# Performance work log

Measured on AMD Instinct MI355X. Metric: run time of the kernel, lower is better.

The kernel has to match this reference:

```python
import jax, jax.numpy as jnp
import numpy as np


def _mlp1(x, W, b):
    return jax.nn.relu(x @ W + b)


def _forward(battle_x, side_x, user_x, moveset_feat, movepool_feat, lookup_move_feat,
             lookup_move_mask, lastberry, lastberry_mask, items, abilities, types_x,
             tera_types_x, opt_moves, move_mask, can_tera, switch_mask,
             W_item, b_item, W_ab, b_ab, W_ms, b_ms, W_user, b_user,
             W_mo1, b_mo1, W_mo2, b_mo2, W_so1, b_so1, W_so2, b_so2,
             active_idx, switch_idx):
    B = battle_x.shape[0]
    # --- user block (vectorized over [B, 2 sides, 6 team members]) ---
    ms = _mlp1(moveset_feat, W_ms, b_ms)                    # [B,2,6,4,128]
    pool = _mlp1(movepool_feat, W_ms, b_ms).mean(axis=-2)   # [B,2,6,128] mean over move pool
    move_set_x = jnp.maximum(ms.max(axis=-2), pool)         # max over [4 slots + pool-mean]
    item_x = _mlp1(items, W_item, b_item).mean(axis=-2)     # [B,2,6,128]
    ability_x = _mlp1(abilities, W_ab, b_ab).mean(axis=-2)  # [B,2,6,128]
    # optional lookup slots: mask*relu(Wx+b) == zero vector when absent
    lk = _mlp1(lookup_move_feat, W_ms, b_ms) * lookup_move_mask[..., None]  # [B,2,6,5,128]
    berry = _mlp1(lastberry, W_item, b_item) * lastberry_mask[..., None]    # [B,2,6,128]
    lk_flat = lk.reshape(B, 2, 6, 5 * 128)
    u_in = jnp.concatenate([user_x, lk_flat, berry, move_set_x, item_x, ability_x,
                            types_x, tera_types_x], axis=-1)                # [B,2,6,1281]
    u = _mlp1(u_in, W_user, b_user)                                         # [B,2,6,512]
    # --- side block ---
    active = jnp.take_along_axis(u, active_idx[:, :, None, None], axis=2)[:, :, 0]  # [B,2,512]
    side_out = jnp.concatenate([side_x, active, u.max(axis=2)], axis=-1)    # [B,2,1041]
    battle_full = jnp.concatenate([battle_x, side_out[:, 0], side_out[:, 1]], axis=-1)  # [B,2091]
    D = battle_full.shape[-1]
    # --- move options: 4 moves x tera in {0,1} ---
    bt = jnp.broadcast_to(battle_full[:, None, None, :], (B, 4, 2, D))
    mv = jnp.broadcast_to(opt_moves[:, :, None, :], (B, 4, 2, 128))
    tera = jnp.broadcast_to(jnp.arange(2, dtype=battle_x.dtype)[None, None, :, None], (B, 4, 2, 1))
    xm = jnp.concatenate([bt, mv, tera], axis=-1)                           # [B,4,2,2220]
    mlogit = (_mlp1(xm, W_mo1, b_mo1) @ W_mo2 + b_mo2)[..., 0]              # [B,4,2]
    tera_ok = jnp.stack([jnp.ones_like(can_tera), can_tera], axis=-1)       # [B,2]
    mvalid = move_mask[:, :, None] * tera_ok[:, None, :]
    mlogit = jnp.where(mvalid > 0, mlogit, -jnp.inf).reshape(B, 8)
    # --- switch options ---
    sw = jnp.take_along_axis(u[:, 0], switch_idx[:, :, None], axis=1)       # [B,6,512]
    xs = jnp.concatenate([jnp.broadcast_to(battle_full[:, None, :], (B, 6, D)), sw], axis=-1)
    slogit = (_mlp1(xs, W_so1, b_so1) @ W_so2 + b_so2)[..., 0]              # [B,6]
    slogit = jnp.where(switch_mask > 0, slogit, -jnp.inf)
    return jnp.concatenate([mlogit, slogit], axis=-1)                       # [B,14]


def setup_inputs() -> dict:
    key = jax.random.key(0)
    ks = jax.random.split(key, 40)
    B = 512
    f32 = jnp.float32
    n = lambda k, s, sc=1.0: jax.random.normal(k, s, f32) * sc
    bern = lambda k, s, p: (jax.random.uniform(k, s) < p).astype(f32)
    inp = {
        'battle_x': n(ks[0], (B, 9)),
        'side_x': n(ks[1], (B, 2, 17)),
        'user_x': n(ks[2], (B, 2, 6, 89)),
        'moveset_feat': n(ks[3], (B, 2, 6, 4, 516)),
        'movepool_feat': n(ks[4], (B, 2, 6, 8, 516)),
        'lookup_move_feat': n(ks[5], (B, 2, 6, 5, 516)),
        'lookup_move_mask': bern(ks[6], (B, 2, 6, 5), 0.5),
        'lastberry': n(ks[7], (B, 2, 6, 256)),
        'lastberry_mask': bern(ks[8], (B, 2, 6), 0.5),
        'items': n(ks[9], (B, 2, 6, 2, 256)),
        'abilities': n(ks[10], (B, 2, 6, 2, 256)),
        'types_x': bern(ks[11], (B, 2, 6, 20), 0.1),
        'tera_types_x': bern(ks[12], (B, 2, 6, 20), 0.1),
        'opt_moves': n(ks[13], (B, 4, 128)),
        'move_mask': bern(ks[14], (B, 4), 0.9),
        'can_tera': bern(ks[15], (B,), 0.5),
        'switch_mask': bern(ks[16], (B, 6), 0.8),
        'W_item': n(ks[17], (256, 128), 0.05), 'b_item': n(ks[18], (128,), 0.05),
        'W_ab': n(ks[19], (256, 128), 0.05), 'b_ab': n(ks[20], (128,), 0.05),
        'W_ms': n(ks[21], (516, 128), 0.05), 'b_ms': n(ks[22], (128,), 0.05),
        'W_user': n(ks[23], (1281, 512), 0.02), 'b_user': n(ks[24], (512,), 0.02),
        'W_mo1': n(ks[25], (2220, 512), 0.02), 'b_mo1': n(ks[26], (512,), 0.02),
        'W_mo2': n(ks[27], (512, 1), 0.05), 'b_mo2': n(ks[28], (1,), 0.05),
        'W_so1': n(ks[29], (2603, 512), 0.02), 'b_so1': n(ks[30], (512,), 0.02),
        'W_so2': n(ks[31], (512, 1), 0.05), 'b_so2': n(ks[32], (1,), 0.05),
        'active_idx': jax.random.randint(ks[33], (B, 2), 0, 6),
        'switch_idx': jax.random.randint(ks[34], (B, 6), 0, 6),
    }
    return inp


def reference(battle_x, side_x, user_x, moveset_feat, movepool_feat, lookup_move_feat,
              lookup_move_mask, lastberry, lastberry_mask, items, abilities, types_x,
              tera_types_x, opt_moves, move_mask, can_tera, switch_mask,
              W_item, b_item, W_ab, b_ab, W_ms, b_ms, W_user, b_user,
              W_mo1, b_mo1, W_mo2, b_mo2, W_so1, b_so1, W_so2, b_so2,
              active_idx, switch_idx):
    return _forward(battle_x, side_x, user_x, moveset_feat, movepool_feat, lookup_move_feat,
                    lookup_move_mask, lastberry, lastberry_mask, items, abilities, types_x,
                    tera_types_x, opt_moves, move_mask, can_tera, switch_mask,
                    W_item, b_item, W_ab, b_ab, W_ms, b_ms, W_user, b_user,
                    W_mo1, b_mo1, W_mo2, b_mo2, W_so1, b_so1, W_so2, b_so2,
                    active_idx, switch_idx)
```

## Files before the change

kernel.cpp:

```cpp
#include <hip/hip_runtime.h>
#include <math.h>

#define BATCH 512
#define NEG_BIG (-3.0e38f)

typedef __attribute__((ext_vector_type(8))) short short8;
typedef __attribute__((ext_vector_type(4))) float floatx4;

__device__ inline unsigned pk2(float lo, float hi) {
    return __builtin_amdgcn_perm(__float_as_uint(hi), __float_as_uint(lo), 0x07060302u);
}
__device__ inline short8 cvt8(float4 a, float4 b) {
    union { unsigned u[4]; short8 s; } r;
    r.u[0] = pk2(a.x, a.y); r.u[1] = pk2(a.z, a.w);
    r.u[2] = pk2(b.x, b.y); r.u[3] = pk2(b.z, b.w);
    return r.s;
}
__device__ inline short f2bf(float f) {
    unsigned u = __float_as_uint(f);
    u += 0x7FFFu + ((u >> 16) & 1u);
    return (short)(u >> 16);
}
__device__ inline float bf2f(short s) {
    return __uint_as_float(((unsigned)(unsigned short)s) << 16);
}

typedef const __attribute__((address_space(1))) unsigned GU32;
typedef __attribute__((address_space(3))) unsigned LU32;
__device__ inline void gload16(const float* g, float* l) {
    __builtin_amdgcn_global_load_lds((GU32*)g, (LU32*)l, 16, 0, 0);
}

__device__ inline void wprep_body(
    const float* __restrict__ W, int K, int N,
    short* __restrict__ Wt, int KP, int k_off,
    int lid, int kbt, float (*tile)[33])
{
    const int kb = (lid % kbt) * 32, nb = (lid / kbt) * 32;
    const int c = threadIdx.x & 31, r0 = threadIdx.x >> 5;
    #pragma unroll
    for (int i = 0; i < 4; ++i) {
        const int r = r0 + i * 8;
        const int k = kb + r;
        tile[r][c] = (k < K) ? W[(size_t)k * N + nb + c] : 0.f;
    }
    __syncthreads();
    #pragma unroll
    for (int i = 0; i < 4; ++i) {
        const int n = nb + r0 + i * 8;
        Wt[(size_t)n * KP + k_off + kb + c] = f2bf(tile[c][r0 + i * 8]);
    }
}

__global__ __launch_bounds__(256) void k_wprep_all(
    const float* __restrict__ W_ms, const float* __restrict__ W_item,
    const float* __restrict__ W_ab, const float* __restrict__ W_user,
    const float* __restrict__ W_mo1, const float* __restrict__ W_so1,
    short* __restrict__ Wt_pre, short* __restrict__ Wt_user,
    short* __restrict__ Wt_mo, short* __restrict__ Wt_mv,
    short* __restrict__ Wt_so, short* __restrict__ Wt_sw)
{
    __shared__ float tile[32][33];
    const int l = blockIdx.x;
    if      (l < 68)   wprep_body(W_ms,   516,  128, Wt_pre,  1056, 0,   l,        17, tile);
    else if (l < 100)  wprep_body(W_item, 256,  128, Wt_pre,  1056, 544, l - 68,   8,  tile);
    else if (l < 132)  wprep_body(W_ab,   256,  128, Wt_pre,  1056, 800, l - 100,  8,  tile);
    else if (l < 788)  wprep_body(W_user, 1281, 512, Wt_user, 1312, 0,   l - 132,  41, tile);
    else if (l < 1844) wprep_body(W_mo1,  2091, 512, Wt_mo,   2112, 0,   l - 788,  66, tile);
    else if (l < 1908) wprep_body(W_mo1 + (size_t)2091 * 512, 128, 512, Wt_mv, 128, 0, l - 1844, 4, tile);
    else if (l < 2964) wprep_body(W_so1,  2091, 512, Wt_so,   2112, 0,   l - 1908, 66, tile);
    else               wprep_body(W_so1 + (size_t)2091 * 512, 512, 512, Wt_sw, 512, 0, l - 2964, 16, tile);
}

#define ASTR 548
#define IOFF 9316
#define ISTR 260
#define ZF   516

__global__ __launch_bounds__(256, 3) void k_pre_gemm(
    const float* __restrict__ moveset, const float* __restrict__ movepool,
    const float* __restrict__ lookup,  const float* __restrict__ items,
    const float* __restrict__ lastberry, const float* __restrict__ abilities,
    const float* __restrict__ lookup_mask, const float* __restrict__ berry_mask,
    const float* __restrict__ user_x, const float* __restrict__ types_x,
    const float* __restrict__ tera_types,
    const short* __restrict__ Wt,
    const float* __restrict__ b_ms, const float* __restrict__ b_item,
    const float* __restrict__ b_ab,
    short* __restrict__ u_in)
{
    __shared__ __align__(16) float Sf[10616];
    const int t = threadIdx.x;
    const int bsu = blockIdx.x;
    const int lane = t & 63, w = t >> 6;

    {
        const int i0 = t, i1 = t + 256;
        if (i0 < 544) Sf[(i0 >> 5) * ASTR + 516 + (i0 & 31)] = 0.f;
        if (i1 < 544) Sf[(i1 >> 5) * ASTR + 516 + (i1 & 31)] = 0.f;
    }

    for (int r = w; r < 17; r += 4) {
        const float* src = (r < 4)  ? moveset  + ((size_t)bsu * 4 + r) * 516
                         : (r < 12) ? movepool + ((size_t)bsu * 8 + (r - 4)) * 516
                                    : lookup   + ((size_t)bsu * 5 + (r - 12)) * 516;
        float* dst = Sf + r * ASTR;
        gload16(src + lane * 4, dst);
        gload16(src + 256 + lane * 4, dst + 256);
        if (lane == 0) gload16(src + 512, dst + 512);
    }
    {
        float* If = Sf + IOFF;
        if (w == 1) {
            gload16(items     + ((size_t)bsu * 2 + 0) * 256 + lane * 4, If + 0 * ISTR);
            gload16(abilities + ((size_t)bsu * 2 + 0) * 256 + lane * 4, If + 3 * ISTR);
        } else if (w == 2) {
            gload16(items     + ((size_t)bsu * 2 + 1) * 256 + lane * 4, If + 1 * ISTR);
            gload16(abilities + ((size_t)bsu * 2 + 1) * 256 + lane * 4, If + 4 * ISTR);
        } else if (w == 3) {
            gload16(lastberry + (size_t)bsu * 256 + lane * 4, If + 2 * ISTR);
        }
    }
    __syncthreads();

    const int m = lane & 15, q = lane >> 4;
    const int aoff = q * 8;

    int t2base = ZF, t2lo = 1, t2hi = 0;
    if (m == 0)      { t2base = 16 * ASTR;              t2lo = 0;  t2hi = 16; }
    else if (m <= 2) { t2base = IOFF + (m - 1) * ISTR;  t2lo = 17; t2hi = 24; }
    else if (m == 3) { t2base = IOFF + 2 * ISTR;        t2lo = 17; t2hi = 24; }
    else if (m <= 5) { t2base = IOFF + (m - 1) * ISTR;  t2lo = 25; t2hi = 32; }

    const short* bp0 = Wt + (size_t)(w * 32 + m) * 1056 + q * 8;
    const short* bp1 = bp0 + (size_t)16 * 1056;

    floatx4 acc[2][2];
    #pragma unroll
    for (int i = 0; i < 2; ++i) {
        acc[i][0] = (floatx4){0.f, 0.f, 0.f, 0.f};
        acc[i][1] = (floatx4){0.f, 0.f, 0.f, 0.f};
    }

    short8 B0[4], B1[4];
    #pragma unroll
    for (int d = 0; d < 4; ++d) {
        B0[d] = *(const short8*)(bp0 + d * 32);
        B1[d] = *(const short8*)(bp1 + d * 32);
    }

    #pragma unroll
    for (int s = 0; s <= 16; ++s) {
        const int k0 = m * ASTR + s * 32 + aoff;
        short8 a0 = cvt8(*(const float4*)(Sf + k0), *(const float4*)(Sf + k0 + 4));
        const int e2 = (s >= t2lo && s <= t2hi) ? t2base + (s - t2lo) * 32 + aoff : ZF;
        short8 a2 = cvt8(*(const float4*)(Sf + e2), *(const float4*)(Sf + e2 + 4));
        acc[0][0] = __builtin_amdgcn_mfma_f32_16x16x32_bf16(a0, B0[s & 3], acc[0][0], 0, 0, 0);
        acc[0][1] = __builtin_amdgcn_mfma_f32_16x16x32_bf16(a0, B1[s & 3], acc[0][1], 0, 0, 0);
        acc[1][0] = __builtin_amdgcn_mfma_f32_16x16x32_bf16(a2, B0[s & 3], acc[1][0], 0, 0, 0);
        acc[1][1] = __builtin_amdgcn_mfma_f32_16x16x32_bf16(a2, B1[s & 3], acc[1][1], 0, 0, 0);
        if (s + 4 <= 32) {
            B0[s & 3] = *(const short8*)(bp0 + (s + 4) * 32);
            B1[s & 3] = *(const short8*)(bp1 + (s + 4) * 32);
        }
    }
    #pragma unroll
    for (int s = 17; s <= 32; ++s) {
        const int e2 = (s >= t2lo && s <= t2hi) ? t2base + (s - t2lo) * 32 + aoff : ZF;
        short8 a2 = cvt8(*(const float4*)(Sf + e2), *(const float4*)(Sf + e2 + 4));
        acc[1][0] = __builtin_amdgcn_mfma_f32_16x16x32_bf16(a2, B0[s & 3], acc[1][0], 0, 0, 0);
        acc[1][1] = __builtin_amdgcn_mfma_f32_16x16x32_bf16(a2, B1[s & 3], acc[1][1], 0, 0, 0);
        if (s + 4 <= 32) {
            B0[s & 3] = *(const short8*)(bp0 + (s + 4) * 32);
            B1[s & 3] = *(const short8*)(bp1 + (s + 4) * 32);
        }
    }

    __syncthreads();
    float* ec = Sf;

    #pragma unroll
    for (int nt = 0; nt < 2; ++nt) {
        const int col = w * 32 + nt * 16 + m;
        #pragma unroll
        for (int r = 0; r < 4; ++r) {
            const int row = q * 4 + r;
            ec[col * 25 + row] = acc[0][nt][r];
            if (row < 6) ec[col * 25 + 16 + row] = acc[1][nt][r];
        }
    }
    __syncthreads();
    if (t < 128) {
        const int c = t;
        const float* v = &ec[c * 25];
        short* __restrict__ orow = u_in + (size_t)bsu * 1312;
        const float bms = b_ms[c], bit = b_item[c], bab = b_ab[c];
        float msx = 0.f;
        #pragma unroll
        for (int r = 0; r < 4; ++r) msx = fmaxf(msx, v[r] + bms);
        float pool = 0.f;
        #pragma unroll
        for (int r = 4; r < 12; ++r) pool += fmaxf(v[r] + bms, 0.f);
        pool *= 0.125f;
        orow[857 + c] = f2bf(fmaxf(msx, pool));
        #pragma unroll
        for (int sl = 0; sl < 5; ++sl) {
            const float mask = lookup_mask[bsu * 5 + sl];
            orow[89 + sl * 128 + c] = f2bf(fmaxf(v[12 + sl] + bms, 0.f) * mask);
        }
        orow[985 + c]  = f2bf(0.5f * (fmaxf(v[17] + bit, 0.f) + fmaxf(v[18] + bit, 0.f)));
        orow[729 + c]  = f2bf(fmaxf(v[19] + bit, 0.f) * berry_mask[bsu]);
        orow[1113 + c] = f2bf(0.5f * (fmaxf(v[20] + bab, 0.f) + fmaxf(v[21] + bab, 0.f)));
        if (c < 89) orow[c] = f2bf(user_x[(size_t)bsu * 89 + c]);
        if (c < 20) {
            orow[1241 + c] = f2bf(types_x[bsu * 20 + c]);
            orow[1261 + c] = f2bf(tera_types[bsu * 20 + c]);
        }
        if (c < 31) orow[1281 + c] = 0;
    }
}

template<int AMODE, bool ABF16, bool RELU, bool HASBIAS, bool OBF16>
__global__ __launch_bounds__(256, 3) void k_gemm(
    const void* __restrict__ Av, int strideA,
    const void* __restrict__ gbasev, const int* __restrict__ gidx,
    const short* __restrict__ Wt, int KP,
    const float* __restrict__ bias,
    void* __restrict__ Cv, size_t partStride, int ksteps)
{
    const int t = threadIdx.x, lane = t & 63, w = t >> 6;
    const int m = lane & 15, q = lane >> 4;
    const int bid = blockIdx.y * gridDim.x + blockIdx.x;
    const int mb = (bid / gridDim.y) * 32;
    const int nb = (bid % gridDim.y) * 128 + w * 32;
    const int z = blockIdx.z;
    const int koff = z * ksteps * 32;

    const short* aps[2]; const float* apf[2];
    #pragma unroll
    for (int i = 0; i < 2; ++i) {
        const int row = mb + i * 16 + m;
        size_t roff;
        if (AMODE == 0) roff = (size_t)row * strideA;
        else {
            const int bb = row / 6, j = row - bb * 6;
            roff = ((size_t)bb * 12 + gidx[bb * 6 + j]) * 512;
        }
        if (ABF16) aps[i] = (const short*)Av + roff + koff + q * 8;
        else       apf[i] = (const float*)Av + roff + koff + q * 8;
        if (AMODE == 1) aps[i] = (const short*)gbasev + roff + koff + q * 8;
    }
    const short* bp0 = Wt + (size_t)(nb + m) * KP + koff + q * 8;
    const short* bp1 = bp0 + (size_t)16 * KP;

    floatx4 acc[2][2];
    #pragma unroll
    for (int i = 0; i < 2; ++i) {
        acc[i][0] = (floatx4){0.f, 0.f, 0.f, 0.f};
        acc[i][1] = (floatx4){0.f, 0.f, 0.f, 0.f};
    }

    short8 Ab[4][2];
    float4 Af[4][2][2];
    short8 B0b[4], B1b[4];
    #pragma unroll
    for (int d = 0; d < 4; ++d) {
        #pragma unroll
        for (int i = 0; i < 2; ++i) {
            if (ABF16) Ab[d][i] = *(const short8*)(aps[i] + d * 32);
            else {
                Af[d][i][0] = *(const float4*)(apf[i] + d * 32);
                Af[d][i][1] = *(const float4*)(apf[i] + d * 32 + 4);
            }
        }
        B0b[d] = *(const short8*)(bp0 + d * 32);
        B1b[d] = *(const short8*)(bp1 + d * 32);
    }

    int s = 0;
    for (; s + 4 < ksteps; s += 4) {
        #pragma unroll
        for (int d = 0; d < 4; ++d) {
            #pragma unroll
            for (int i = 0; i < 2; ++i) {
                const short8 av = ABF16 ? Ab[d][i] : cvt8(Af[d][i][0], Af[d][i][1]);
                acc[i][0] = __builtin_amdgcn_mfma_f32_16x16x32_bf16(av, B0b[d], acc[i][0], 0, 0, 0);
                acc[i][1] = __builtin_amdgcn_mfma_f32_16x16x32_bf16(av, B1b[d], acc[i][1], 0, 0, 0);
            }
            int ns = s + d + 4; if (ns > ksteps - 1) ns = ksteps - 1;
            const int o = ns * 32;
            #pragma unroll
            for (int i = 0; i < 2; ++i) {
                if (ABF16) Ab[d][i] = *(const short8*)(aps[i] + o);
                else {
                    Af[d][i][0] = *(const float4*)(apf[i] + o);
                    Af[d][i][1] = *(const float4*)(apf[i] + o + 4);
                }
            }
            B0b[d] = *(const short8*)(bp0 + o);
            B1b[d] = *(const short8*)(bp1 + o);
        }
    }
    #pragma unroll
    for (int d = 0; d < 4; ++d) {
        if (s + d < ksteps) {
            #pragma unroll
            for (int i = 0; i < 2; ++i) {
                const short8 av = ABF16 ? Ab[d][i] : cvt8(Af[d][i][0], Af[d][i][1]);
                acc[i][0] = __builtin_amdgcn_mfma_f32_16x16x32_bf16(av, B0b[d], acc[i][0], 0, 0, 0);
                acc[i][1] = __builtin_amdgcn_mfma_f32_16x16x32_bf16(av, B1b[d], acc[i][1], 0, 0, 0);
            }
        }
    }

    const float bb0 = (HASBIAS && z == 0) ? bias[nb + m] : 0.f;
    const float bb1 = (HASBIAS && z == 0) ? bias[nb + 16 + m] : 0.f;
    #pragma unroll
    for (int i = 0; i < 2; ++i) {
        #pragma unroll
        for (int r = 0; r < 4; ++r) {
            const int row = mb + i * 16 + q * 4 + r;
            float v0 = acc[i][0][r] + bb0;
            float v1 = acc[i][1][r] + bb1;
            if (RELU) { v0 = fmaxf(v0, 0.f); v1 = fmaxf(v1, 0.f); }
            if (OBF16) {
                short* C = (short*)Cv + z * partStride;
                C[(size_t)row * 512 + nb + m]      = f2bf(v0);
                C[(size_t)row * 512 + nb + 16 + m] = f2bf(v1);
            } else {
                float* C = (float*)Cv + z * partStride;
                C[(size_t)row * 512 + nb + m]      = v0;
                C[(size_t)row * 512 + nb + 16 + m] = v1;
            }
        }
    }
}

__global__ __launch_bounds__(256) void k_battle(
    const float* __restrict__ battle_x, const float* __restrict__ side_x,
    const short* __restrict__ u, const int* __restrict__ active_idx,
    short* __restrict__ bfb)
{
    const int b = blockIdx.x;
    const int t = threadIdx.x;
    short* __restrict__ o = bfb + (size_t)b * 2112;
    if (t < 9) o[t] = f2bf(battle_x[b * 9 + t]);
    if (t < 21) o[2091 + t] = 0;
    for (int s = 0; s < 2; ++s) {
        const short* __restrict__ us = u + (size_t)(b * 2 + s) * 6 * 512;
        const int act = active_idx[b * 2 + s];
        if (t < 17) o[9 + s * 1041 + t] = f2bf(side_x[(b * 2 + s) * 17 + t]);
        for (int c = t; c < 512; c += 256) {
            float mx = bf2f(us[c]);
            #pragma unroll
            for (int uu = 1; uu < 6; ++uu) mx = fmaxf(mx, bf2f(us[uu * 512 + c]));
            o[9 + s * 1041 + 17 + c]       = us[act * 512 + c];
            o[9 + s * 1041 + 17 + 512 + c] = f2bf(mx);
        }
    }
}

__global__ __launch_bounds__(512) void k_epi_mo(
    const float* __restrict__ C_mo, size_t partStride, int nparts,
    const float* __restrict__ D_mv,
    const float* __restrict__ W1, const float* __restrict__ W2,
    const float* __restrict__ b2,
    const float* __restrict__ move_mask, const float* __restrict__ can_tera,
    float* __restrict__ out)
{
    __shared__ float red[8][8];
    const int b = blockIdx.x, t = threadIdx.x;
    float h = 0.f;
    for (int p = 0; p < nparts; ++p) h += C_mo[p * partStride + (size_t)b * 512 + t];
    const float wt = W1[(size_t)2219 * 512 + t];
    const float w2 = W2[t];
    float dm[4];
    #pragma unroll
    for (int m = 0; m < 4; ++m) dm[m] = D_mv[((size_t)b * 4 + m) * 512 + t];
    const int lane = t & 63, wid = t >> 6;
    #pragma unroll
    for (int m = 0; m < 4; ++m) {
        #pragma unroll
        for (int tt = 0; tt < 2; ++tt) {
            float hv = fmaxf(h + dm[m] + (tt ? wt : 0.f), 0.f);
            float v = hv * w2;
            #pragma unroll
            for (int off = 32; off > 0; off >>= 1) v += __shfl_down(v, off);
            if (lane == 0) red[m * 2 + tt][wid] = v;
        }
    }
    __syncthreads();
    if (t < 8) {
        float s = 0.f;
        #pragma unroll
        for (int ww = 0; ww < 8; ++ww) s += red[t][ww];
        s += b2[0];
        const int m = t >> 1, tt = t & 1;
        const float ok = move_mask[b * 4 + m] * (tt ? can_tera[b] : 1.f);
        out[b * 14 + t] = (ok > 0.f) ? s : NEG_BIG;
    }
}

__global__ __launch_bounds__(512) void k_epi_sw(
    const float* __restrict__ C_so, size_t partStride, int nparts,
    const float* __restrict__ D_sw,
    const float* __restrict__ W2, const float* __restrict__ b2,
    const float* __restrict__ switch_mask, float* __restrict__ out)
{
    __shared__ float red[6][8];
    const int b = blockIdx.x, t = threadIdx.x;
    float h = 0.f;
    for (int p = 0; p < nparts; ++p) h += C_so[p * partStride + (size_t)b * 512 + t];
    const float w2 = W2[t];
    const int lane = t & 63, wid = t >> 6;
    #pragma unroll
    for (int j = 0; j < 6; ++j) {
        float hv = fmaxf(h + D_sw[((size_t)b * 6 + j) * 512 + t], 0.f);
        float v = hv * w2;
        #pragma unroll
        for (int off = 32; off > 0; off >>= 1) v += __shfl_down(v, off);
        if (lane == 0) red[j][wid] = v;
    }
    __syncthreads();
    if (t < 6) {
        float s = 0.f;
        #pragma unroll
        for (int ww = 0; ww < 8; ++ww) s += red[t][ww];
        s += b2[0];
        out[b * 14 + 8 + t] = (switch_mask[b * 6 + t] > 0.f) ? s : NEG_BIG;
    }
}

extern "C" void kernel_launch(void* const* d_in, const int* in_sizes, int n_in,
                              void* d_out, int out_size, void* d_ws, size_t ws_size,
                              hipStream_t stream) {
    const float* battle_x    = (const float*)d_in[0];
    const float* side_x      = (const float*)d_in[1];
    const float* user_x      = (const float*)d_in[2];
    const float* moveset     = (const float*)d_in[3];
    const float* movepool    = (const float*)d_in[4];
    const float* lookup      = (const float*)d_in[5];
    const float* lookup_mask = (const float*)d_in[6];
    const float* lastberry   = (const float*)d_in[7];
    const float* berry_mask  = (const float*)d_in[8];
    const float* items       = (const float*)d_in[9];
    const float* abilities   = (const float*)d_in[10];
    const float* types_x     = (const float*)d_in[11];
    const float* tera_types  = (const float*)d_in[12];
    const float* opt_moves   = (const float*)d_in[13];
    const float* move_mask   = (const float*)d_in[14];
    const float* can_tera    = (const float*)d_in[15];
    const float* switch_mask = (const float*)d_in[16];
    const float* W_item = (const float*)d_in[17];
    const float* b_item = (const float*)d_in[18];
    const float* W_ab   = (const float*)d_in[19];
    const float* b_ab   = (const float*)d_in[20];
    const float* W_ms   = (const float*)d_in[21];
    const float* b_ms   = (const float*)d_in[22];
    const float* W_user = (const float*)d_in[23];
    const float* b_user = (const float*)d_in[24];
    const float* W_mo1  = (const float*)d_in[25];
    const float* b_mo1  = (const float*)d_in[26];
    const float* W_mo2  = (const float*)d_in[27];
    const float* b_mo2  = (const float*)d_in[28];
    const float* W_so1  = (const float*)d_in[29];
    const float* b_so1  = (const float*)d_in[30];
    const float* W_so2  = (const float*)d_in[31];
    const float* b_so2  = (const float*)d_in[32];
    const int* active_idx = (const int*)d_in[33];
    const int* switch_idx = (const int*)d_in[34];
    float* out = (float*)d_out;

    char* base = (char*)d_ws;
    size_t off = 0;
    short* u_in = (short*)(base + off); off += (size_t)6144 * 1312 * 2;
    short* u    = (short*)(base + off); off += (size_t)6144 * 512 * 2;
    short* bfb  = (short*)(base + off); off += (size_t)512 * 2112 * 2;
    float* C_mo = (float*)(base + off); off += (size_t)6 * 512 * 512 * 4;
    float* C_so = (float*)(base + off); off += (size_t)6 * 512 * 512 * 4;
    float* D_mv = (float*)(base + off); off += (size_t)2048 * 512 * 4;
    float* D_sw = (float*)(base + off); off += (size_t)3072 * 512 * 4;
    short* Wt_pre  = (short*)(base + off); off += (size_t)128 * 1056 * 2;
    short* Wt_user = (short*)(base + off); off += (size_t)512 * 1312 * 2;
    short* Wt_mo   = (short*)(base + off); off += (size_t)512 * 2112 * 2;
    short* Wt_so   = (short*)(base + off); off += (size_t)512 * 2112 * 2;
    short* Wt_mv   = (short*)(base + off); off += (size_t)512 * 128 * 2;
    short* Wt_sw   = (short*)(base + off); off += (size_t)512 * 512 * 2;

    k_wprep_all<<<3220, 256, 0, stream>>>(W_ms, W_item, W_ab, W_user, W_mo1, W_so1,
                                          Wt_pre, Wt_user, Wt_mo, Wt_mv, Wt_so, Wt_sw);

    k_pre_gemm<<<6144, 256, 0, stream>>>(moveset, movepool, lookup, items, lastberry,
                                         abilities, lookup_mask, berry_mask,
                                         user_x, types_x, tera_types,
                                         Wt_pre, b_ms, b_item, b_ab, u_in);
    k_gemm<0, true, true, true, true><<<dim3(192, 4, 1), 256, 0, stream>>>(
        u_in, 1312, nullptr, nullptr, Wt_user, 1312, b_user, u, 0, 41);
    k_battle<<<BATCH, 256, 0, stream>>>(battle_x, side_x, u, active_idx, bfb);
    k_gemm<0, true, false, true, false><<<dim3(16, 4, 6), 256, 0, stream>>>(
        bfb, 2112, nullptr, nullptr, Wt_mo, 2112, b_mo1, C_mo, (size_t)512 * 512, 11);
    k_gemm<0, false, false, false, false><<<dim3(64, 4, 1), 256, 0, stream>>>(
        opt_moves, 128, nullptr, nullptr, Wt_mv, 128, nullptr, D_mv, 0, 4);
    k_gemm<0, true, false, true, false><<<dim3(16, 4, 6), 256, 0, stream>>>(
        bfb, 2112, nullptr, nullptr, Wt_so, 2112, b_so1, C_so, (size_t)512 * 512, 11);
    k_gemm<1, true, false, false, false><<<dim3(96, 4, 1), 256, 0, stream>>>(
        nullptr, 0, u, switch_idx, Wt_sw, 512, nullptr, D_sw, 0, 16);
    k_epi_mo<<<BATCH, 512, 0, stream>>>(C_mo, (size_t)512 * 512, 6, D_mv, W_mo1,
                                        W_mo2, b_mo2, move_mask, can_tera, out);
    k_epi_sw<<<BATCH, 512, 0, stream>>>(C_so, (size_t)512 * 512, 6, D_sw,
                                        W_so2, b_so2, switch_mask, out);
}
```

Before: 535.6 us.

## Make pre-GEMM kernel persistent with double-buffered LDS staging across rows

Converts k_pre_gemm from one block per (batch, side, member) row to 256 persistent blocks that each process 24 rows. The next row's inputs are loaded into a second LDS buffer while the current row's MFMA work runs. This hides global load latency and amortizes per-block setup. In exchange it uses one block per CU with double LDS, which lowers occupancy, and the full vmcnt(0) wait at the top of each iteration may limit how much overlap is actually achieved.

```diff
diff --git a/kernel.cpp b/kernel.cpp
--- a/kernel.cpp
+++ b/kernel.cpp
@@ -76,8 +76,9 @@
 #define IOFF 9316
 #define ISTR 260
 #define ZF   516
-
-__global__ __launch_bounds__(256, 3) void k_pre_gemm(
+#define BUFW 10616
+
+__global__ __launch_bounds__(256, 1) void k_pre_gemm(
     const float* __restrict__ moveset, const float* __restrict__ movepool,
     const float* __restrict__ lookup,  const float* __restrict__ items,
     const float* __restrict__ lastberry, const float* __restrict__ abilities,
@@ -89,28 +90,22 @@
     const float* __restrict__ b_ab,
     short* __restrict__ u_in)
 {
-    __shared__ __align__(16) float Sf[10616];
+    __shared__ __align__(16) float Sf[2 * BUFW];
     const int t = threadIdx.x;
-    const int bsu = blockIdx.x;
     const int lane = t & 63, w = t >> 6;
-
-    {
-        const int i0 = t, i1 = t + 256;
-        if (i0 < 544) Sf[(i0 >> 5) * ASTR + 516 + (i0 & 31)] = 0.f;
-        if (i1 < 544) Sf[(i1 >> 5) * ASTR + 516 + (i1 & 31)] = 0.f;
-    }
-
-    for (int r = w; r < 17; r += 4) {
-        const float* src = (r < 4)  ? moveset  + ((size_t)bsu * 4 + r) * 516
-                         : (r < 12) ? movepool + ((size_t)bsu * 8 + (r - 4)) * 516
-                                    : lookup   + ((size_t)bsu * 5 + (r - 12)) * 516;
-        float* dst = Sf + r * ASTR;
-        gload16(src + lane * 4, dst);
-        gload16(src + 256 + lane * 4, dst + 256);
-        if (lane == 0) gload16(src + 512, dst + 512);
-    }
-    {
-        float* If = Sf + IOFF;
+    const int bsu_base = blockIdx.x * 24;
+
+    auto stage = [&](int bsu, float* dstbuf) {
+        for (int r = w; r < 17; r += 4) {
+            const float* src = (r < 4)  ? moveset  + ((size_t)bsu * 4 + r) * 516
+                             : (r < 12) ? movepool + ((size_t)bsu * 8 + (r - 4)) * 516
+                                        : lookup   + ((size_t)bsu * 5 + (r - 12)) * 516;
+            float* dst = dstbuf + r * ASTR;
+            gload16(src + lane * 4, dst);
+            gload16(src + 256 + lane * 4, dst + 256);
+            if (lane == 0) gload16(src + 512, dst + 512);
+        }
+        float* If = dstbuf + IOFF;
         if (w == 1) {
             gload16(items     + ((size_t)bsu * 2 + 0) * 256 + lane * 4, If + 0 * ISTR);
             gload16(abilities + ((size_t)bsu * 2 + 0) * 256 + lane * 4, If + 3 * ISTR);
@@ -120,103 +115,123 @@
         } else if (w == 3) {
             gload16(lastberry + (size_t)bsu * 256 + lane * 4, If + 2 * ISTR);
         }
-    }
-    __syncthreads();
+    };
+
+    for (int i = t; i < 1088; i += 256) {
+        const int b = i / 544, j = i - b * 544;
+        Sf[b * BUFW + (j >> 5) * ASTR + 516 + (j & 31)] = 0.f;
+    }
 
     const int m = lane & 15, q = lane >> 4;
     const int aoff = q * 8;
-
     int t2base = ZF, t2lo = 1, t2hi = 0;
-    if (m == 0)      { t2base = 16 * ASTR;              t2lo = 0;  t2hi = 16; }
-    else if (m <= 2) { t2base = IOFF + (m - 1) * ISTR;  t2lo = 17; t2hi = 24; }
-    else if (m == 3) { t2base = IOFF + 2 * ISTR;        t2lo = 17; t2hi = 24; }
-    else if (m <= 5) { t2base = IOFF + (m - 1) * ISTR;  t2lo = 25; t2hi = 32; }
+    if (m == 0)      { t2base = 16 * ASTR;             t2lo = 0;  t2hi = 16; }
+    else if (m <= 2) { t2base = IOFF + (m - 1) * ISTR; t2lo = 17; t2hi = 24; }
+    else if (m == 3) { t2base = IOFF + 2 * ISTR;       t2lo = 17; t2hi = 24; }
+    else if (m <= 5) { t2base = IOFF + (m - 1) * ISTR; t2lo = 25; t2hi = 32; }
 
     const short* bp0 = Wt + (size_t)(w * 32 + m) * 1056 + q * 8;
     const short* bp1 = bp0 + (size_t)16 * 1056;
 
-    floatx4 acc[2][2];
-    #pragma unroll
-    for (int i = 0; i < 2; ++i) {
-        acc[i][0] = (floatx4){0.f, 0.f, 0.f, 0.f};
-        acc[i][1] = (floatx4){0.f, 0.f, 0.f, 0.f};
-    }
-
-    short8 B0[4], B1[4];
-    #pragma unroll
-    for (int d = 0; d < 4; ++d) {
-        B0[d] = *(const short8*)(bp0 + d * 32);
-        B1[d] = *(const short8*)(bp1 + d * 32);
-    }
-
-    #pragma unroll
-    for (int s = 0; s <= 16; ++s) {
-        const int k0 = m * ASTR + s * 32 + aoff;
-        short8 a0 = cvt8(*(const float4*)(Sf + k0), *(const float4*)(Sf + k0 + 4));
-        const int e2 = (s >= t2lo && s <= t2hi) ? t2base + (s - t2lo) * 32 + aoff : ZF;
-        short8 a2 = cvt8(*(const float4*)(Sf + e2), *(const float4*)(Sf + e2 + 4));
-        acc[0][0] = __builtin_amdgcn_mfma_f32_16x16x32_bf16(a0, B0[s & 3], acc[0][0], 0, 0, 0);
-        acc[0][1] = __builtin_amdgcn_mfma_f32_16x16x32_bf16(a0, B1[s & 3], acc[0][1], 0, 0, 0);
-        acc[1][0] = __builtin_amdgcn_mfma_f32_16x16x32_bf16(a2, B0[s & 3], acc[1][0], 0, 0, 0);
-        acc[1][1] = __builtin_amdgcn_mfma_f32_16x16x32_bf16(a2, B1[s & 3], acc[1][1], 0, 0, 0);
-        if (s + 4 <= 32) {
-            B0[s & 3] = *(const short8*)(bp0 + (s + 4) * 32);
-            B1[s & 3] = *(const short8*)(bp1 + (s + 4) * 32);
-        }
-    }
-    #pragma unroll
-    for (int s = 17; s <= 32; ++s) {
-        const int e2 = (s >= t2lo && s <= t2hi) ? t2base + (s - t2lo) * 32 + aoff : ZF;
-        short8 a2 = cvt8(*(const float4*)(Sf + e2), *(const float4*)(Sf + e2 + 4));
-        acc[1][0] = __builtin_amdgcn_mfma_f32_16x16x32_bf16(a2, B0[s & 3], acc[1][0], 0, 0, 0);
-        acc[1][1] = __builtin_amdgcn_mfma_f32_16x16x32_bf16(a2, B1[s & 3], acc[1][1], 0, 0, 0);
-        if (s + 4 <= 32) {
-            B0[s & 3] = *(const short8*)(bp0 + (s + 4) * 32);
-            B1[s & 3] = *(const short8*)(bp1 + (s + 4) * 32);
-        }
-    }
-
-    __syncthreads();
-    float* ec = Sf;
-
-    #pragma unroll
-    for (int nt = 0; nt < 2; ++nt) {
-        const int col = w * 32 + nt * 16 + m;
-        #pragma unroll
-        for (int r = 0; r < 4; ++r) {
-            const int row = q * 4 + r;
-            ec[col * 25 + row] = acc[0][nt][r];
-            if (row < 6) ec[col * 25 + 16 + row] = acc[1][nt][r];
-        }
-    }
-    __syncthreads();
-    if (t < 128) {
-        const int c = t;
-        const float* v = &ec[c * 25];
-        short* __restrict__ orow = u_in + (size_t)bsu * 1312;
-        const float bms = b_ms[c], bit = b_item[c], bab = b_ab[c];
-        float msx = 0.f;
-        #pragma unroll
-        for (int r = 0; r < 4; ++r) msx = fmaxf(msx, v[r] + bms);
-        float pool = 0.f;
-        #pragma unroll
-        for (int r = 4; r < 12; ++r) pool += fmaxf(v[r] + bms, 0.f);
-        pool *= 0.125f;
-        orow[857 + c] = f2bf(fmaxf(msx, pool));
-        #pragma unroll
-        for (int sl = 0; sl < 5; ++sl) {
-            const float mask = lookup_mask[bsu * 5 + sl];
-            orow[89 + sl * 128 + c] = f2bf(fmaxf(v[12 + sl] + bms, 0.f) * mask);
-        }
-        orow[985 + c]  = f2bf(0.5f * (fmaxf(v[17] + bit, 0.f) + fmaxf(v[18] + bit, 0.f)));
-        orow[729 + c]  = f2bf(fmaxf(v[19] + bit, 0.f) * berry_mask[bsu]);
-        orow[1113 + c] = f2bf(0.5f * (fmaxf(v[20] + bab, 0.f) + fmaxf(v[21] + bab, 0.f)));
-        if (c < 89) orow[c] = f2bf(user_x[(size_t)bsu * 89 + c]);
-        if (c < 20) {
-            orow[1241 + c] = f2bf(types_x[bsu * 20 + c]);
-            orow[1261 + c] = f2bf(tera_types[bsu * 20 + c]);
-        }
-        if (c < 31) orow[1281 + c] = 0;
+    stage(bsu_base, Sf);
+
+    #pragma unroll 2
+    for (int it = 0; it < 24; ++it) {
+        const int bsu = bsu_base + it;
+        float* buf = Sf + (it & 1) * BUFW;
+
+        asm volatile("s_waitcnt vmcnt(0) lgkmcnt(0)" ::: "memory");
+        __builtin_amdgcn_sched_barrier(0);
+        __builtin_amdgcn_s_barrier();
+
+        floatx4 acc[2][2];
+        #pragma unroll
+        for (int i = 0; i < 2; ++i) {
+            acc[i][0] = (floatx4){0.f, 0.f, 0.f, 0.f};
+            acc[i][1] = (floatx4){0.f, 0.f, 0.f, 0.f};
+        }
+        short8 B0[4], B1[4];
+        #pragma unroll
+        for (int d = 0; d < 4; ++d) {
+            B0[d] = *(const short8*)(bp0 + d * 32);
+            B1[d] = *(const short8*)(bp1 + d * 32);
+        }
+        #pragma unroll
+        for (int s = 0; s <= 16; ++s) {
+            const int k0 = m * ASTR + s * 32 + aoff;
+            short8 a0 = cvt8(*(const float4*)(buf + k0), *(const float4*)(buf + k0 + 4));
+            const int e2 = (s >= t2lo && s <= t2hi) ? t2base + (s - t2lo) * 32 + aoff : ZF;
+            short8 a2 = cvt8(*(const float4*)(buf + e2), *(const float4*)(buf + e2 + 4));
+            acc[0][0] = __builtin_amdgcn_mfma_f32_16x16x32_bf16(a0, B0[s & 3], acc[0][0], 0, 0, 0);
+            acc[0][1] = __builtin_amdgcn_mfma_f32_16x16x32_bf16(a0, B1[s & 3], acc[0][1], 0, 0, 0);
+            acc[1][0] = __builtin_amdgcn_mfma_f32_16x16x32_bf16(a2, B0[s & 3], acc[1][0], 0, 0, 0);
+            acc[1][1] = __builtin_amdgcn_mfma_f32_16x16x32_bf16(a2, B1[s & 3], acc[1][1], 0, 0, 0);
+            if (s + 4 <= 32) {
+                B0[s & 3] = *(const short8*)(bp0 + (s + 4) * 32);
+                B1[s & 3] = *(const short8*)(bp1 + (s + 4) * 32);
+            }
+        }
+        #pragma unroll
+        for (int s = 17; s <= 32; ++s) {
+            const int e2 = (s >= t2lo && s <= t2hi) ? t2base + (s - t2lo) * 32 + aoff : ZF;
+            short8 a2 = cvt8(*(const float4*)(buf + e2), *(const float4*)(buf + e2 + 4));
+            acc[1][0] = __builtin_amdgcn_mfma_f32_16x16x32_bf16(a2, B0[s & 3], acc[1][0], 0, 0, 0);
+            acc[1][1] = __builtin_amdgcn_mfma_f32_16x16x32_bf16(a2, B1[s & 3], acc[1][1], 0, 0, 0);
+            if (s + 4 <= 32) {
+                B0[s & 3] = *(const short8*)(bp0 + (s + 4) * 32);
+                B1[s & 3] = *(const short8*)(bp1 + (s + 4) * 32);
+            }
+        }
+
+        if (it + 1 < 24) stage(bsu + 1, Sf + ((it + 1) & 1) * BUFW);
+
+        asm volatile("s_waitcnt lgkmcnt(0)" ::: "memory");
+        __builtin_amdgcn_sched_barrier(0);
+        __builtin_amdgcn_s_barrier();
+
+        float* ec = buf;
+        #pragma unroll
+        for (int nt = 0; nt < 2; ++nt) {
+            const int col = w * 32 + nt * 16 + m;
+            #pragma unroll
+            for (int r = 0; r < 4; ++r) {
+                const int row = q * 4 + r;
+                ec[col * 25 + row] = acc[0][nt][r];
+                if (row < 6) ec[col * 25 + 16 + row] = acc[1][nt][r];
+            }
+        }
+        asm volatile("s_waitcnt lgkmcnt(0)" ::: "memory");
+        __builtin_amdgcn_sched_barrier(0);
+        __builtin_amdgcn_s_barrier();
+
+        if (t < 128) {
+            const int c = t;
+            const float* v = &ec[c * 25];
+            short* __restrict__ orow = u_in + (size_t)bsu * 1312;
+            const float bms = b_ms[c], bit = b_item[c], bab = b_ab[c];
+            float msx = 0.f;
+            #pragma unroll
+            for (int r = 0; r < 4; ++r) msx = fmaxf(msx, v[r] + bms);
+            float pool = 0.f;
+            #pragma unroll
+            for (int r = 4; r < 12; ++r) pool += fmaxf(v[r] + bms, 0.f);
+            pool *= 0.125f;
+            orow[857 + c] = f2bf(fmaxf(msx, pool));
+            #pragma unroll
+            for (int sl = 0; sl < 5; ++sl) {
+                const float mask = lookup_mask[bsu * 5 + sl];
+                orow[89 + sl * 128 + c] = f2bf(fmaxf(v[12 + sl] + bms, 0.f) * mask);
+            }
+            orow[985 + c]  = f2bf(0.5f * (fmaxf(v[17] + bit, 0.f) + fmaxf(v[18] + bit, 0.f)));
+            orow[729 + c]  = f2bf(fmaxf(v[19] + bit, 0.f) * berry_mask[bsu]);
+            orow[1113 + c] = f2bf(0.5f * (fmaxf(v[20] + bab, 0.f) + fmaxf(v[21] + bab, 0.f)));
+            if (c < 89) orow[c] = f2bf(user_x[(size_t)bsu * 89 + c]);
+            if (c < 20) {
+                orow[1241 + c] = f2bf(types_x[bsu * 20 + c]);
+                orow[1261 + c] = f2bf(tera_types[bsu * 20 + c]);
+            }
+            if (c < 31) orow[1281 + c] = 0;
+        }
     }
 }
 
@@ -490,10 +505,10 @@
     k_wprep_all<<<3220, 256, 0, stream>>>(W_ms, W_item, W_ab, W_user, W_mo1, W_so1,
                                           Wt_pre, Wt_user, Wt_mo, Wt_mv, Wt_so, Wt_sw);
 
-    k_pre_gemm<<<6144, 256, 0, stream>>>(moveset, movepool, lookup, items, lastberry,
-                                         abilities, lookup_mask, berry_mask,
-                                         user_x, types_x, tera_types,
-                                         Wt_pre, b_ms, b_item, b_ab, u_in);
+    k_pre_gemm<<<256, 256, 0, stream>>>(moveset, movepool, lookup, items, lastberry,
+                                        abilities, lookup_mask, berry_mask,
+                                        user_x, types_x, tera_types,
+                                        Wt_pre, b_ms, b_item, b_ab, u_in);
     k_gemm<0, true, true, true, true><<<dim3(192, 4, 1), 256, 0, stream>>>(
         u_in, 1312, nullptr, nullptr, Wt_user, 1312, b_user, u, 0, 41);
     k_battle<<<BATCH, 256, 0, stream>>>(battle_x, side_x, u, active_idx, bfb);
```

Result: slower. 551.0 us (+2.9%).
